# Kernel tuning notes

Hardware: AMD Instinct MI355X
Metric: run time of the kernel (lower is better)

Reference implementation:

```python
import jax, jax.numpy as jnp
import numpy as np

LAPLACIAN = jnp.array([[-1., -1., -1.], [-1., 8., -1.], [-1., -1., -1.]], dtype=jnp.float32).reshape(1, 1, 3, 3)
AVG5 = jnp.ones((1, 1, 5, 5), dtype=jnp.float32) / 25.0


def _conv_same(x, kernel):
    # x: [B,1,H,W], kernel: [O=1,I=1,kh,kw], SAME padding (odd kernels)
    return jax.lax.conv_general_dilated(
        x, kernel, window_strides=(1, 1), padding='SAME',
        dimension_numbers=('NCHW', 'OIHW', 'NCHW'))


def setup_inputs() -> dict:
    key = jax.random.key(0)
    k0, k1, k2, k3 = jax.random.split(key, 4)
    B, H, W = 16, 1024, 1024
    mask = jax.random.uniform(k0, (B, 1, H, W), dtype=jnp.float32)
    # per-sample params scaled into documented ranges
    blur_strength = 1.0 + 4.0 * jax.random.uniform(k1, (B, 1), dtype=jnp.float32)      # 1.0-5.0
    edge_sensitivity = 0.5 + 1.5 * jax.random.uniform(k2, (B, 1), dtype=jnp.float32)   # 0.5-2.0
    final_threshold = 0.3 + 0.4 * jax.random.uniform(k3, (B, 1), dtype=jnp.float32)    # 0.3-0.7
    return {"mask": mask, "blur_strength": blur_strength,
            "edge_sensitivity": edge_sensitivity, "final_threshold": final_threshold}


def reference(mask, blur_strength, edge_sensitivity, final_threshold):
    B = mask.shape[0]
    edges = jnp.abs(_conv_same(mask, LAPLACIAN))                      # [B,1,H,W]
    edge_threshold = 0.5 * edge_sensitivity.reshape(B, 1, 1, 1)
    edge_mask = (edges > edge_threshold).astype(mask.dtype)
    smoothed_base = _conv_same(mask, AVG5)                            # 5x5 box blur
    blur_factor = blur_strength.reshape(B, 1, 1, 1) / 3.0
    smoothed = mask * (1.0 - blur_factor) + smoothed_base * blur_factor
    result = mask * (1.0 - edge_mask) + smoothed * edge_mask
    final_mask = (result > final_threshold.reshape(B, 1, 1, 1)).astype(mask.dtype)
    return final_mask
```

## Files before the change

### kernel.cpp

```cpp
#include <hip/hip_runtime.h>

#define NB 16
#define HH 1024
#define WW 1024
#define TW 128
#define TH 32
#define LC 136
#define LR 36
#define N4 (LR * (LC / 4))

#define EPS1 2e-4f
#define EPS2 1e-4f

__device__ __noinline__ float aes_exact(const float (*raw)[LC], int lr, int lc,
                                        float bsf, float esf, float fthr)
{
    const double bfd   = (double)bsf / 3.0;
    const double ethrd = 0.5 * (double)esf;
    const double fthrd = (double)fthr;
    const double w25d  = (double)(1.0f / 25.0f);

    double s25 = 0.0, s9 = 0.0;
    for (int dy = 0; dy < 5; ++dy)
        for (int dx = 0; dx < 5; ++dx) {
            double v = (double)raw[lr + dy][lc + dx];
            s25 += v;
            if (dy >= 1 && dy <= 3 && dx >= 1 && dx <= 3) s9 += v;
        }
    double c      = (double)raw[lr + 2][lc + 2];
    double edges  = fabs(9.0 * c - s9);
    double sbase  = s25 * w25d;
    double smooth = c * (1.0 - bfd) + sbase * bfd;
    double result = (edges > ethrd) ? smooth : c;
    return (result > fthrd) ? 1.0f : 0.0f;
}

__global__ __launch_bounds__(256)
void aes_kernel(const float* __restrict__ mask,
                const float* __restrict__ blur_strength,
                const float* __restrict__ edge_sensitivity,
                const float* __restrict__ final_threshold,
                float* __restrict__ out)
{
    __shared__ float raw[LR][LC];

    const int b      = blockIdx.z;
    const int tile_x = blockIdx.x * TW;
    const int tile_y = blockIdx.y * TH;
    const float* m = mask + (size_t)b * (HH * WW);

    for (int i = threadIdx.x; i < N4; i += 256) {
        int row = i / (LC / 4);
        int c4  = i - row * (LC / 4);
        int gy  = tile_y - 2 + row;
        int gx  = tile_x - 4 + 4 * c4;
        float4 v = make_float4(0.f, 0.f, 0.f, 0.f);
        if ((unsigned)gy < (unsigned)HH && (unsigned)gx < (unsigned)WW)
            v = *(const float4*)(m + (size_t)gy * WW + gx);
        *(float4*)&raw[row][4 * c4] = v;
    }
    __syncthreads();

    const float bsf    = blur_strength[b];
    const float esf    = edge_sensitivity[b];
    const float fthr   = final_threshold[b];
    const float ethr   = 0.5f * esf;
    const float bff    = bsf / 3.0f;
    const float onembf = 1.0f - bff;
    const float w25f   = 1.0f / 25.0f;

    const int tx  = threadIdx.x & 31;
    const int ty  = threadIdx.x >> 5;
    const int lr0 = ty * 4;
    const int lc0 = 4 * tx + 2;

    float h5[5][4], h3[5][4], cc[5][4];

#define LOADROW(ROWIDX, K)                                                  \
    {                                                                       \
        const float* rp = &raw[(ROWIDX)][0];                                \
        float2 u0 = *(const float2*)(rp + lc0);            \
        float4 u1 = *(const float4*)(rp + lc0 + 2);        \
        float2 u2 = *(const float2*)(rp + lc0 + 6);        \
        float a0 = u0.x, a1 = u0.y, a2 = u1.x, a3 = u1.y;                   \
        float a4 = u1.z, a5 = u1.w, a6 = u2.x, a7 = u2.y;                   \
        float s5 = ((a0 + a1) + (a2 + a3)) + a4;                            \
        h5[(K)][0] = s5; s5 = s5 - a0 + a5;                                 \
        h5[(K)][1] = s5; s5 = s5 - a1 + a6;                                 \
        h5[(K)][2] = s5; s5 = s5 - a2 + a7;                                 \
        h5[(K)][3] = s5;                                                    \
        float s3 = (a1 + a2) + a3;                                          \
        h3[(K)][0] = s3; s3 = s3 - a1 + a4;                                 \
        h3[(K)][1] = s3; s3 = s3 - a2 + a5;                                 \
        h3[(K)][2] = s3; s3 = s3 - a3 + a6;                                 \
        h3[(K)][3] = s3;                                                    \
        cc[(K)][0] = a2; cc[(K)][1] = a3; cc[(K)][2] = a4; cc[(K)][3] = a5; \
    }

    #pragma unroll
    for (int k = 0; k < 4; ++k)
        LOADROW(lr0 + k, k)

    float* op = out + (size_t)b * (HH * WW)
                    + (size_t)(tile_y + ty * 4) * WW + tile_x + 4 * tx;

    #pragma unroll
    for (int r = 0; r < 4; ++r) {
        LOADROW(lr0 + r + 4, (r + 4) % 5)
        const int i0 = r % 5, i1 = (r + 1) % 5, i2 = (r + 2) % 5;
        const int i3 = (r + 3) % 5, i4 = (r + 4) % 5;

        float4 ov;
        #pragma unroll
        for (int c = 0; c < 4; ++c) {
            float sum25  = ((h5[i0][c] + h5[i1][c]) + (h5[i2][c] + h5[i3][c])) + h5[i4][c];
            float s9     = h3[i1][c] + h3[i2][c] + h3[i3][c];
            float center = cc[i2][c];

            float edges  = fabsf(9.0f * center - s9);
            float sbase  = sum25 * w25f;
            float smooth = center * onembf + sbase * bff;

            bool isedge = edges > ethr;
            bool conf = (fabsf(edges - ethr) > EPS1) &&
                        (!isedge || (fabsf(smooth - fthr) > EPS2));
            float res = isedge ? smooth : center;
            float o   = (res > fthr) ? 1.0f : 0.0f;

            if (!conf)
                o = aes_exact(raw, lr0 + r, lc0 + c, bsf, esf, fthr);

            (&ov.x)[c] = o;
        }
        *(float4*)(op + (size_t)r * WW) = ov;
    }
#undef LOADROW
}

extern "C" void kernel_launch(void* const* d_in, const int* in_sizes, int n_in,
                              void* d_out, int out_size, void* d_ws, size_t ws_size,
                              hipStream_t stream) {
    const float* mask = (const float*)d_in[0];
    const float* bs   = (const float*)d_in[1];
    const float* es   = (const float*)d_in[2];
    const float* ft   = (const float*)d_in[3];
    float* out = (float*)d_out;

    dim3 grid(WW / TW, HH / TH, NB);
    aes_kernel<<<grid, 256, 0, stream>>>(mask, bs, es, ft, out);
}
```

Measured before the change: 37.74 us.

## Drop LDS staging, read stencil rows directly from global, taller tiles

Removes the shared-memory tile and its barrier, so each thread loads its 5-row sliding window straight from global memory and relies on the cache to share halo rows between neighbours. The tile height doubles so each thread produces 8 rows instead of 4, which lowers the vertical halo overhead. Output stores become nontemporal, and the double-precision fallback now reads from global memory. The cost is more global and cache traffic per output element, plus extra boundary checks on every load.

```diff
diff --git a/kernel.cpp b/kernel.cpp
--- a/kernel.cpp
+++ b/kernel.cpp
@@ -4,16 +4,16 @@
 #define HH 1024
 #define WW 1024
 #define TW 128
-#define TH 32
-#define LC 136
-#define LR 36
-#define N4 (LR * (LC / 4))
+#define TH 64
 
 #define EPS1 2e-4f
 #define EPS2 1e-4f
 
-__device__ __noinline__ float aes_exact(const float (*raw)[LC], int lr, int lc,
-                                        float bsf, float esf, float fthr)
+typedef float f32x4 __attribute__((ext_vector_type(4)));
+
+__device__ __noinline__ float aes_exact_g(const float* __restrict__ m,
+                                          int gy, int gx,
+                                          float bsf, float esf, float fthr)
 {
     const double bfd   = (double)bsf / 3.0;
     const double ethrd = 0.5 * (double)esf;
@@ -21,13 +21,16 @@
     const double w25d  = (double)(1.0f / 25.0f);
 
     double s25 = 0.0, s9 = 0.0;
-    for (int dy = 0; dy < 5; ++dy)
-        for (int dx = 0; dx < 5; ++dx) {
-            double v = (double)raw[lr + dy][lc + dx];
+    for (int dy = -2; dy <= 2; ++dy)
+        for (int dx = -2; dx <= 2; ++dx) {
+            int yy = gy + dy, xx = gx + dx;
+            double v = 0.0;
+            if ((unsigned)yy < (unsigned)HH && (unsigned)xx < (unsigned)WW)
+                v = (double)m[(size_t)yy * WW + xx];
             s25 += v;
-            if (dy >= 1 && dy <= 3 && dx >= 1 && dx <= 3) s9 += v;
+            if (dy >= -1 && dy <= 1 && dx >= -1 && dx <= 1) s9 += v;
         }
-    double c      = (double)raw[lr + 2][lc + 2];
+    double c      = (double)m[(size_t)gy * WW + gx];
     double edges  = fabs(9.0 * c - s9);
     double sbase  = s25 * w25d;
     double smooth = c * (1.0 - bfd) + sbase * bfd;
@@ -42,24 +45,10 @@
                 const float* __restrict__ final_threshold,
                 float* __restrict__ out)
 {
-    __shared__ float raw[LR][LC];
-
     const int b      = blockIdx.z;
     const int tile_x = blockIdx.x * TW;
     const int tile_y = blockIdx.y * TH;
     const float* m = mask + (size_t)b * (HH * WW);
-
-    for (int i = threadIdx.x; i < N4; i += 256) {
-        int row = i / (LC / 4);
-        int c4  = i - row * (LC / 4);
-        int gy  = tile_y - 2 + row;
-        int gx  = tile_x - 4 + 4 * c4;
-        float4 v = make_float4(0.f, 0.f, 0.f, 0.f);
-        if ((unsigned)gy < (unsigned)HH && (unsigned)gx < (unsigned)WW)
-            v = *(const float4*)(m + (size_t)gy * WW + gx);
-        *(float4*)&raw[row][4 * c4] = v;
-    }
-    __syncthreads();
 
     const float bsf    = blur_strength[b];
     const float esf    = edge_sensitivity[b];
@@ -69,19 +58,29 @@
     const float onembf = 1.0f - bff;
     const float w25f   = 1.0f / 25.0f;
 
-    const int tx  = threadIdx.x & 31;
-    const int ty  = threadIdx.x >> 5;
-    const int lr0 = ty * 4;
-    const int lc0 = 4 * tx + 2;
+    const int tx = threadIdx.x & 31;
+    const int ty = threadIdx.x >> 5;
+    const int x0 = tile_x + 4 * tx;
+    const int y0 = tile_y + 8 * ty;
+
+    const bool lok = (x0 > 0);
+    const bool rok = (x0 < WW - 4);
 
     float h5[5][4], h3[5][4], cc[5][4];
 
-#define LOADROW(ROWIDX, K)                                                  \
+#define LOADROW(GY, K)                                                      \
     {                                                                       \
-        const float* rp = &raw[(ROWIDX)][0];                                \
-        float2 u0 = *(const float2*)(rp + lc0);            \
-        float4 u1 = *(const float4*)(rp + lc0 + 2);        \
-        float2 u2 = *(const float2*)(rp + lc0 + 6);        \
+        const int gy_ = (GY);                                               \
+        const float* rp = m + (size_t)gy_ * WW + x0;                        \
+        const bool rv = (unsigned)gy_ < (unsigned)HH;                       \
+        float2 u0 = make_float2(0.f, 0.f);                                  \
+        float4 u1 = make_float4(0.f, 0.f, 0.f, 0.f);                        \
+        float2 u2 = make_float2(0.f, 0.f);                                  \
+        if (rv) {                                                           \
+            if (lok) u0 = *(const float2*)(rp - 2);        \
+            u1 = *(const float4*)rp;                       \
+            if (rok) u2 = *(const float2*)(rp + 4);        \
+        }                                                                   \
         float a0 = u0.x, a1 = u0.y, a2 = u1.x, a3 = u1.y;                   \
         float a4 = u1.z, a5 = u1.w, a6 = u2.x, a7 = u2.y;                   \
         float s5 = ((a0 + a1) + (a2 + a3)) + a4;                            \
@@ -99,18 +98,17 @@
 
     #pragma unroll
     for (int k = 0; k < 4; ++k)
-        LOADROW(lr0 + k, k)
+        LOADROW(y0 - 2 + k, k)
 
-    float* op = out + (size_t)b * (HH * WW)
-                    + (size_t)(tile_y + ty * 4) * WW + tile_x + 4 * tx;
+    float* op = out + (size_t)b * (HH * WW) + (size_t)y0 * WW + x0;
 
     #pragma unroll
-    for (int r = 0; r < 4; ++r) {
-        LOADROW(lr0 + r + 4, (r + 4) % 5)
+    for (int r = 0; r < 8; ++r) {
+        LOADROW(y0 + 2 + r, (r + 4) % 5)
         const int i0 = r % 5, i1 = (r + 1) % 5, i2 = (r + 2) % 5;
         const int i3 = (r + 3) % 5, i4 = (r + 4) % 5;
 
-        float4 ov;
+        f32x4 ov;
         #pragma unroll
         for (int c = 0; c < 4; ++c) {
             float sum25  = ((h5[i0][c] + h5[i1][c]) + (h5[i2][c] + h5[i3][c])) + h5[i4][c];
@@ -128,11 +126,11 @@
             float o   = (res > fthr) ? 1.0f : 0.0f;
 
             if (!conf)
-                o = aes_exact(raw, lr0 + r, lc0 + c, bsf, esf, fthr);
+                o = aes_exact_g(m, y0 + r, x0 + c, bsf, esf, fthr);
 
-            (&ov.x)[c] = o;
+            ov[c] = o;
         }
-        *(float4*)(op + (size_t)r * WW) = ov;
+        __builtin_nontemporal_store(ov, (f32x4*)(op + (size_t)r * WW));
     }
 #undef LOADROW
 }
```

New measurement: 78.35 us. 2.08x slower.

## Process two tiles per block with register-staged double-buffered shared memory

Applied to the files above, without the earlier changes.

Each block now handles two adjacent 128-wide tiles. The global loads for the second tile are issued into registers while the first tile is being computed, then written into a second shared-memory buffer. The aim is to hide global-load latency behind stencil compute. Output stores now use nontemporal stores. In exchange, shared memory per block doubles, register pressure rises from the staging registers, and the grid is halved, which may lower occupancy.

```diff
diff --git a/kernel.cpp b/kernel.cpp
--- a/kernel.cpp
+++ b/kernel.cpp
@@ -8,9 +8,12 @@
 #define LC 136
 #define LR 36
 #define N4 (LR * (LC / 4))
+#define NSTG 5
 
 #define EPS1 2e-4f
 #define EPS2 1e-4f
+
+typedef float f32x4 __attribute__((ext_vector_type(4)));
 
 __device__ __noinline__ float aes_exact(const float (*raw)[LC], int lr, int lc,
                                         float bsf, float esf, float fthr)
@@ -42,24 +45,12 @@
                 const float* __restrict__ final_threshold,
                 float* __restrict__ out)
 {
-    __shared__ float raw[LR][LC];
+    __shared__ float raw[2][LR][LC];
 
     const int b      = blockIdx.z;
-    const int tile_x = blockIdx.x * TW;
     const int tile_y = blockIdx.y * TH;
+    const int tx0    = blockIdx.x * (2 * TW);
     const float* m = mask + (size_t)b * (HH * WW);
-
-    for (int i = threadIdx.x; i < N4; i += 256) {
-        int row = i / (LC / 4);
-        int c4  = i - row * (LC / 4);
-        int gy  = tile_y - 2 + row;
-        int gx  = tile_x - 4 + 4 * c4;
-        float4 v = make_float4(0.f, 0.f, 0.f, 0.f);
-        if ((unsigned)gy < (unsigned)HH && (unsigned)gx < (unsigned)WW)
-            v = *(const float4*)(m + (size_t)gy * WW + gx);
-        *(float4*)&raw[row][4 * c4] = v;
-    }
-    __syncthreads();
 
     const float bsf    = blur_strength[b];
     const float esf    = edge_sensitivity[b];
@@ -74,11 +65,42 @@
     const int lr0 = ty * 4;
     const int lc0 = 4 * tx + 2;
 
-    float h5[5][4], h3[5][4], cc[5][4];
+    f32x4 stg[NSTG];
 
-#define LOADROW(ROWIDX, K)                                                  \
+#define STAGE_LOAD(TILE_X)                                                  \
     {                                                                       \
-        const float* rp = &raw[(ROWIDX)][0];                                \
+        _Pragma("unroll")                                                   \
+        for (int k = 0; k < NSTG; ++k) {                                    \
+            int i = (int)threadIdx.x + k * 256;                             \
+            f32x4 v = {0.f, 0.f, 0.f, 0.f};                                 \
+            if (i < N4) {                                                   \
+                int row = i / (LC / 4);                                     \
+                int c4  = i - row * (LC / 4);                               \
+                int gy  = tile_y - 2 + row;                                 \
+                int gx  = (TILE_X) - 4 + 4 * c4;           \
+                if ((unsigned)gy < (unsigned)HH && (unsigned)gx < (unsigned)WW) \
+                    v = *(const f32x4*)(m + (size_t)gy * WW + gx);          \
+            }                                                               \
+            stg[k] = v;                                                     \
+        }                                                                   \
+    }
+
+#define STAGE_WRITE(BUF)                                                    \
+    {                                                                       \
+        _Pragma("unroll")                                                   \
+        for (int k = 0; k < NSTG; ++k) {                                    \
+            int i = (int)threadIdx.x + k * 256;                             \
+            if (i < N4) {                                                   \
+                int row = i / (LC / 4);                                     \
+                int c4  = i - row * (LC / 4);                               \
+                *(f32x4*)&raw[(BUF)][row][4 * c4] = stg[k];                 \
+            }                                                               \
+        }                                                                   \
+    }
+
+#define LOADROW(RB, ROWIDX, K)                                              \
+    {                                                                       \
+        const float* rp = &RB[(ROWIDX)][0];                                 \
         float2 u0 = *(const float2*)(rp + lc0);            \
         float4 u1 = *(const float4*)(rp + lc0 + 2);        \
         float2 u2 = *(const float2*)(rp + lc0 + 6);        \
@@ -97,44 +119,58 @@
         cc[(K)][0] = a2; cc[(K)][1] = a3; cc[(K)][2] = a4; cc[(K)][3] = a5; \
     }
 
-    #pragma unroll
-    for (int k = 0; k < 4; ++k)
-        LOADROW(lr0 + k, k)
+#define COMPUTE(BUF, TILE_X)                                                \
+    {                                                                       \
+        const float (*rb)[LC] = raw[(BUF)];                                 \
+        float h5[5][4], h3[5][4], cc[5][4];                                 \
+        _Pragma("unroll")                                                   \
+        for (int k = 0; k < 4; ++k)                                         \
+            LOADROW(rb, lr0 + k, k)                                         \
+        float* op = out + (size_t)b * (HH * WW)                             \
+                        + (size_t)(tile_y + ty * 4) * WW + (TILE_X) + 4 * tx; \
+        _Pragma("unroll")                                                   \
+        for (int r = 0; r < 4; ++r) {                                       \
+            LOADROW(rb, lr0 + r + 4, (r + 4) % 5)                           \
+            const int i0 = r % 5, i1 = (r + 1) % 5, i2 = (r + 2) % 5;       \
+            const int i3 = (r + 3) % 5, i4 = (r + 4) % 5;                   \
+            f32x4 ov;                                                       \
+            _Pragma("unroll")                                               \
+            for (int c = 0; c < 4; ++c) {                                   \
+                float sum25  = ((h5[i0][c] + h5[i1][c])                     \
+                              + (h5[i2][c] + h5[i3][c])) + h5[i4][c];       \
+                float s9     = h3[i1][c] + h3[i2][c] + h3[i3][c];           \
+                float center = cc[i2][c];                                   \
+                float edges  = fabsf(9.0f * center - s9);                   \
+                float sbase  = sum25 * w25f;                                \
+                float smooth = center * onembf + sbase * bff;               \
+                bool isedge = edges > ethr;                                 \
+                bool conf = (fabsf(edges - ethr) > EPS1) &&                 \
+                            (!isedge || (fabsf(smooth - fthr) > EPS2));     \
+                float res = isedge ? smooth : center;                       \
+                float o   = (res > fthr) ? 1.0f : 0.0f;                     \
+                if (!conf)                                                  \
+                    o = aes_exact(rb, lr0 + r, lc0 + c, bsf, esf, fthr);    \
+                ov[c] = o;                                                  \
+            }                                                               \
+            __builtin_nontemporal_store(ov, (f32x4*)(op + (size_t)r * WW)); \
+        }                                                                   \
+    }
 
-    float* op = out + (size_t)b * (HH * WW)
-                    + (size_t)(tile_y + ty * 4) * WW + tile_x + 4 * tx;
+    STAGE_LOAD(tx0)
+    STAGE_WRITE(0)
+    __syncthreads();
 
-    #pragma unroll
-    for (int r = 0; r < 4; ++r) {
-        LOADROW(lr0 + r + 4, (r + 4) % 5)
-        const int i0 = r % 5, i1 = (r + 1) % 5, i2 = (r + 2) % 5;
-        const int i3 = (r + 3) % 5, i4 = (r + 4) % 5;
+    STAGE_LOAD(tx0 + TW)
+    COMPUTE(0, tx0)
+    STAGE_WRITE(1)
+    __syncthreads();
 
-        float4 ov;
-        #pragma unroll
-        for (int c = 0; c < 4; ++c) {
-            float sum25  = ((h5[i0][c] + h5[i1][c]) + (h5[i2][c] + h5[i3][c])) + h5[i4][c];
-            float s9     = h3[i1][c] + h3[i2][c] + h3[i3][c];
-            float center = cc[i2][c];
+    COMPUTE(1, tx0 + TW)
 
-            float edges  = fabsf(9.0f * center - s9);
-            float sbase  = sum25 * w25f;
-            float smooth = center * onembf + sbase * bff;
-
-            bool isedge = edges > ethr;
-            bool conf = (fabsf(edges - ethr) > EPS1) &&
-                        (!isedge || (fabsf(smooth - fthr) > EPS2));
-            float res = isedge ? smooth : center;
-            float o   = (res > fthr) ? 1.0f : 0.0f;
-
-            if (!conf)
-                o = aes_exact(raw, lr0 + r, lc0 + c, bsf, esf, fthr);
-
-            (&ov.x)[c] = o;
-        }
-        *(float4*)(op + (size_t)r * WW) = ov;
-    }
+#undef STAGE_LOAD
+#undef STAGE_WRITE
 #undef LOADROW
+#undef COMPUTE
 }
 
 extern "C" void kernel_launch(void* const* d_in, const int* in_sizes, int n_in,
@@ -146,6 +182,6 @@
     const float* ft   = (const float*)d_in[3];
     float* out = (float*)d_out;
 
-    dim3 grid(WW / TW, HH / TH, NB);
+    dim3 grid(WW / (2 * TW), HH / TH, NB);
     aes_kernel<<<grid, 256, 0, stream>>>(mask, bs, es, ft, out);
 }
```

After: 36.49 us. -3.3%, faster.
